# Kernel optimization log

Hardware: AMD Instinct MI355X
Metric: run time of the kernel (lower is better)

The kernel has to match this reference:

```python
import jax, jax.numpy as jnp
import numpy as np

N = 100000
E = 1600000
F_IN = 128
H = 128
C = 2


def setup_inputs() -> dict:
    key = jax.random.key(0)
    ks = jax.random.split(key, 12)
    s = lambda fan_in: 1.0 / np.sqrt(fan_in)
    inp = {
        "x": jax.random.normal(ks[0], (N, F_IN), dtype=jnp.float32),
        "edge_index": jax.random.randint(ks[1], (2, E), 0, N, dtype=jnp.int32),
        "edge_weight": jax.random.uniform(ks[2], (E,), dtype=jnp.float32),
        # first_lin: features_num -> hidden
        "W_first": jax.random.uniform(ks[3], (F_IN, H), minval=-s(F_IN), maxval=s(F_IN)),
        "b_first": jnp.zeros((H,), jnp.float32),
        # GRUCell (torch layout: [3*H, H] for ih and hh)
        "W_ih": jax.random.uniform(ks[4], (3 * H, H), minval=-s(H), maxval=s(H)),
        "b_ih": jax.random.uniform(ks[5], (3 * H,), minval=-s(H), maxval=s(H)),
        "W_hh": jax.random.uniform(ks[6], (3 * H, H), minval=-s(H), maxval=s(H)),
        "b_hh": jax.random.uniform(ks[7], (3 * H,), minval=-s(H), maxval=s(H)),
        # lin1: hidden -> hidden
        "W_lin1": jax.random.uniform(ks[8], (H, H), minval=-s(H), maxval=s(H)),
        "b_lin1": jnp.zeros((H,), jnp.float32),
        # out: hidden -> num_class
        "W_out": jax.random.uniform(ks[9], (H, C), minval=-s(H), maxval=s(H)),
        "b_out": jnp.zeros((C,), jnp.float32),
    }
    return inp


def _gated_conv(x, edge_index, edge_weight):
    # gather source node features, scale by edge weight, scatter-add to dst
    src, dst = edge_index[0], edge_index[1]
    msg = x[src] * edge_weight[:, None]           # [E, H]
    return jax.ops.segment_sum(msg, dst, num_segments=N)  # [N, H]


def _gru_cell(inp, hid, W_ih, b_ih, W_hh, b_hh):
    gi = inp @ W_ih.T + b_ih                      # [N, 3H]
    gh = hid @ W_hh.T + b_hh                      # [N, 3H]
    i_r, i_z, i_n = jnp.split(gi, 3, axis=-1)
    h_r, h_z, h_n = jnp.split(gh, 3, axis=-1)
    r = jax.nn.sigmoid(i_r + h_r)
    z = jax.nn.sigmoid(i_z + h_z)
    n = jnp.tanh(i_n + r * h_n)
    return (1.0 - z) * n + z * hid


def reference(x, edge_index, edge_weight, W_first, b_first, W_ih, b_ih,
              W_hh, b_hh, W_lin1, b_lin1, W_out, b_out):
    x = x @ W_first + b_first                     # [N, H] (dropout: eval mode no-op)
    h = x
    x = _gated_conv(x, edge_index, edge_weight)
    x = _gru_cell(x, h, W_ih, b_ih, W_hh, b_hh)
    x = x @ W_lin1 + b_lin1
    x = _gated_conv(x, edge_index, edge_weight)
    x = _gru_cell(x, h, W_ih, b_ih, W_hh, b_hh)
    logits = x @ W_out + b_out                    # [N, C]
    return jax.nn.log_softmax(logits, axis=-1)
```

## Files before the change

### kernel.cpp

```cpp
#include <hip/hip_runtime.h>
#include <hip/hip_bf16.h>

#define H 128
#define SCAN_T 256
#define SCAN_I 8
#define SCAN_CHUNK (SCAN_T * SCAN_I)

typedef __bf16 bf16_t;
typedef __attribute__((ext_vector_type(2))) __bf16 bf16x2;
typedef __attribute__((ext_vector_type(8))) __bf16 bf16x8;
typedef __attribute__((ext_vector_type(4))) float f32x4;

static_assert(sizeof(bf16x8) == 16, "bf16x8 must be 16 bytes");

__device__ inline bf16x8 load_a_frag_f32(const float* __restrict__ A, int row, int koff) {
    const float4* p = (const float4*)(A + (size_t)row * H + koff);
    float4 v0 = p[0], v1 = p[1];
    bf16x8 r;
    r[0] = (bf16_t)v0.x; r[1] = (bf16_t)v0.y; r[2] = (bf16_t)v0.z; r[3] = (bf16_t)v0.w;
    r[4] = (bf16_t)v1.x; r[5] = (bf16_t)v1.y; r[6] = (bf16_t)v1.z; r[7] = (bf16_t)v1.w;
    return r;
}

__global__ void prep_weights(const float* __restrict__ Wf,  const float* __restrict__ Wih,
                             const float* __restrict__ Whh, const float* __restrict__ Wl1,
                             bf16_t* __restrict__ wfT, bf16_t* __restrict__ wih,
                             bf16_t* __restrict__ whh, bf16_t* __restrict__ wl1T) {
    int i = blockIdx.x * blockDim.x + threadIdx.x;
    if (i < 128 * 128) {
        int c = i >> 7, k = i & 127;
        wfT[i]  = (bf16_t)Wf[k * 128 + c];
        wl1T[i] = (bf16_t)Wl1[k * 128 + c];
    }
    if (i < 384 * 128) {
        wih[i] = (bf16_t)Wih[i];
        whh[i] = (bf16_t)Whh[i];
    }
}

__global__ void hist_kernel(const int* __restrict__ ei, int* __restrict__ deg, int nE) {
    int e = blockIdx.x * blockDim.x + threadIdx.x;
    if (e < nE) atomicAdd(&deg[ei[nE + e]], 1);
}

__global__ __launch_bounds__(SCAN_T) void scan1_kernel(
    const int* __restrict__ deg, int* __restrict__ rowptr, int* __restrict__ bsum, int n) {
    __shared__ int s[SCAN_T];
    int base = blockIdx.x * SCAN_CHUNK + threadIdx.x * SCAN_I;
    int v[SCAN_I];
    int sum = 0;
    for (int j = 0; j < SCAN_I; ++j) {
        int idx = base + j;
        v[j] = (idx < n) ? deg[idx] : 0;
        sum += v[j];
    }
    s[threadIdx.x] = sum;
    __syncthreads();
    for (int off = 1; off < SCAN_T; off <<= 1) {
        int t = (threadIdx.x >= off) ? s[threadIdx.x - off] : 0;
        __syncthreads();
        s[threadIdx.x] += t;
        __syncthreads();
    }
    int run = s[threadIdx.x] - sum;
    for (int j = 0; j < SCAN_I; ++j) {
        int idx = base + j;
        if (idx < n) rowptr[idx] = run;
        run += v[j];
    }
    if (threadIdx.x == SCAN_T - 1) bsum[blockIdx.x] = s[SCAN_T - 1];
}

__global__ __launch_bounds__(SCAN_T) void scan2_kernel(int* __restrict__ bsum, int nb) {
    __shared__ int s[SCAN_T];
    int v = (threadIdx.x < nb) ? bsum[threadIdx.x] : 0;
    s[threadIdx.x] = v;
    __syncthreads();
    for (int off = 1; off < SCAN_T; off <<= 1) {
        int t = (threadIdx.x >= off) ? s[threadIdx.x - off] : 0;
        __syncthreads();
        s[threadIdx.x] += t;
        __syncthreads();
    }
    if (threadIdx.x < nb) bsum[threadIdx.x] = s[threadIdx.x] - v;
}

__global__ void scan3_kernel(int* __restrict__ rowptr, int* __restrict__ cursor,
                             const int* __restrict__ bsum, int n, int nE) {
    int idx = blockIdx.x * blockDim.x + threadIdx.x;
    if (idx < n) {
        int val = rowptr[idx] + bsum[idx / SCAN_CHUNK];
        rowptr[idx] = val;
        cursor[idx] = val;
    }
    if (idx == 0) rowptr[n] = nE;
}

__global__ void scatter_kernel(const int* __restrict__ ei, const float* __restrict__ ew,
                               int* __restrict__ cursor, int2* __restrict__ srcw, int nE) {
    int e = blockIdx.x * blockDim.x + threadIdx.x;
    if (e < nE) {
        int src = ei[e], dst = ei[nE + e];
        float w = ew[e];
        int pos = atomicAdd(&cursor[dst], 1);
        srcw[pos] = make_int2(src, __float_as_int(w));
    }
}

__device__ inline void conv_fma(float* acc, uint4 u, float w) {
    acc[0] += __uint_as_float(u.x << 16) * w;
    acc[1] += __uint_as_float(u.x & 0xffff0000u) * w;
    acc[2] += __uint_as_float(u.y << 16) * w;
    acc[3] += __uint_as_float(u.y & 0xffff0000u) * w;
    acc[4] += __uint_as_float(u.z << 16) * w;
    acc[5] += __uint_as_float(u.z & 0xffff0000u) * w;
    acc[6] += __uint_as_float(u.w << 16) * w;
    acc[7] += __uint_as_float(u.w & 0xffff0000u) * w;
}

__global__ __launch_bounds__(256) void conv_csr_kernel(
    const bf16_t* __restrict__ xb, const int* __restrict__ rowptr,
    const int2* __restrict__ srcw, bf16_t* __restrict__ agg, int n) {
    int lane = threadIdx.x & 63;
    int d = (blockIdx.x * blockDim.x + threadIdx.x) >> 6;
    if (d >= n) return;
    int q = lane >> 4;
    int l = lane & 15;
    int beg = rowptr[d], end = rowptr[d + 1];

    float acc[8];
    #pragma unroll
    for (int i = 0; i < 8; ++i) acc[i] = 0.f;

    int e = beg + q;
    for (; e + 4 < end; e += 8) {
        int2 sw0 = srcw[e];
        int2 sw1 = srcw[e + 4];
        uint4 u0 = *(const uint4*)(xb + (size_t)sw0.x * H + l * 8);
        uint4 u1 = *(const uint4*)(xb + (size_t)sw1.x * H + l * 8);
        conv_fma(acc, u0, __int_as_float(sw0.y));
        conv_fma(acc, u1, __int_as_float(sw1.y));
    }
    if (e < end) {
        int2 sw = srcw[e];
        uint4 u = *(const uint4*)(xb + (size_t)sw.x * H + l * 8);
        conv_fma(acc, u, __int_as_float(sw.y));
    }

    #pragma unroll
    for (int i = 0; i < 8; ++i) {
        acc[i] += __shfl_xor(acc[i], 16);
        acc[i] += __shfl_xor(acc[i], 32);
    }
    if (q == 0) {
        bf16x8 r;
        #pragma unroll
        for (int i = 0; i < 8; ++i) r[i] = (bf16_t)acc[i];
        *(bf16x8*)(agg + (size_t)d * H + l * 8) = r;
    }
}


__global__ __launch_bounds__(256) void lin_first_kernel(
    const float* __restrict__ A, const bf16_t* __restrict__ Bt,
    const float* __restrict__ bias, float* __restrict__ outf,
    bf16_t* __restrict__ outb, int n) {
    __shared__ __align__(16) unsigned char wlds[32768];
    int tid = threadIdx.x;
    int wid = tid >> 6, lane = tid & 63;
    int r0 = (blockIdx.x * 4 + wid) * 32;
    int lrow = lane & 15, lq = lane >> 4, lk8 = lq * 8;

    #pragma unroll
    for (int i = 0; i < 8; ++i) {
        int g = i * 256 + tid;
        int row = g >> 4, seg = g & 15;
        uint4 v = *(const uint4*)(Bt + row * 128 + seg * 8);
        *(uint4*)(&wlds[row * 256 + ((seg * 16) ^ ((row & 7) << 4))]) = v;
    }

    bf16x8 a[2][4];
    for (int rt = 0; rt < 2; ++rt) {
        int row = r0 + rt * 16 + lrow;
        if (row >= n) row = n - 1;
        for (int t = 0; t < 4; ++t) a[rt][t] = load_a_frag_f32(A, row, t * 32 + lk8);
    }
    __syncthreads();

    for (int ct = 0; ct < 8; ++ct) {
        int c0 = ct * 16;
        f32x4 acc0 = {0.f, 0.f, 0.f, 0.f}, acc1 = {0.f, 0.f, 0.f, 0.f};
        int rbase = (c0 + lrow) * 256;
        int sw = (lrow & 7) << 4;
        #pragma unroll
        for (int t = 0; t < 4; ++t) {
            bf16x8 b = *(const bf16x8*)(&wlds[rbase + ((t * 64 + lq * 16) ^ sw)]);
            acc0 = __builtin_amdgcn_mfma_f32_16x16x32_bf16(a[0][t], b, acc0, 0, 0, 0);
            acc1 = __builtin_amdgcn_mfma_f32_16x16x32_bf16(a[1][t], b, acc1, 0, 0, 0);
        }
        int col = c0 + lrow;
        float bv = bias[col];
        for (int r = 0; r < 4; ++r) {
            int row0 = r0 + lq * 4 + r;
            float v0 = acc0[r] + bv;
            if (row0 < n) { outf[(size_t)row0 * H + col] = v0; outb[(size_t)row0 * H + col] = (bf16_t)v0; }
            int row1 = row0 + 16;
            float v1 = acc1[r] + bv;
            if (row1 < n) { outf[(size_t)row1 * H + col] = v1; outb[(size_t)row1 * H + col] = (bf16_t)v1; }
        }
    }
}

__global__ __launch_bounds__(256) void lin_mid_kernel(
    const bf16_t* __restrict__ A, const bf16_t* __restrict__ Bt,
    const float* __restrict__ bias, bf16_t* __restrict__ out, int n) {
    __shared__ __align__(16) unsigned char wlds[32768];
    int tid = threadIdx.x;
    int wid = tid >> 6, lane = tid & 63;
    int r0 = (blockIdx.x * 4 + wid) * 32;
    int lrow = lane & 15, lq = lane >> 4, lk8 = lq * 8;

    #pragma unroll
    for (int i = 0; i < 8; ++i) {
        int g = i * 256 + tid;
        int row = g >> 4, seg = g & 15;
        uint4 v = *(const uint4*)(Bt + row * 128 + seg * 8);
        *(uint4*)(&wlds[row * 256 + ((seg * 16) ^ ((row & 7) << 4))]) = v;
    }

    bf16x8 a[2][4];
    for (int rt = 0; rt < 2; ++rt) {
        int row = r0 + rt * 16 + lrow;
        if (row >= n) row = n - 1;
        for (int t = 0; t < 4; ++t)
            a[rt][t] = *(const bf16x8*)(A + (size_t)row * H + t * 32 + lk8);
    }
    __syncthreads();

    for (int ct = 0; ct < 8; ++ct) {
        int c0 = ct * 16;
        f32x4 acc0 = {0.f, 0.f, 0.f, 0.f}, acc1 = {0.f, 0.f, 0.f, 0.f};
        int rbase = (c0 + lrow) * 256;
        int sw = (lrow & 7) << 4;
        #pragma unroll
        for (int t = 0; t < 4; ++t) {
            bf16x8 b = *(const bf16x8*)(&wlds[rbase + ((t * 64 + lq * 16) ^ sw)]);
            acc0 = __builtin_amdgcn_mfma_f32_16x16x32_bf16(a[0][t], b, acc0, 0, 0, 0);
            acc1 = __builtin_amdgcn_mfma_f32_16x16x32_bf16(a[1][t], b, acc1, 0, 0, 0);
        }
        int col = c0 + lrow;
        float bv = bias[col];
        for (int r = 0; r < 4; ++r) {
            int row0 = r0 + lq * 4 + r;
            if (row0 < n) out[(size_t)row0 * H + col] = (bf16_t)(acc0[r] + bv);
            int row1 = row0 + 16;
            if (row1 < n) out[(size_t)row1 * H + col] = (bf16_t)(acc1[r] + bv);
        }
    }
}

template<bool LOGITS>
__global__ __launch_bounds__(256) void gru_kernel(
    const bf16_t* __restrict__ inp, const bf16_t* __restrict__ hidb,
    const float* __restrict__ hidf,
    const bf16_t* __restrict__ Wih, const bf16_t* __restrict__ Whh,
    const float* __restrict__ bih, const float* __restrict__ bhh,
    bf16_t* __restrict__ out, const float* __restrict__ Wo,
    const float* __restrict__ bo, float* __restrict__ logits, int n) {
    __shared__ __align__(16) unsigned char wlds[2][6 * 4096];
    int tid = threadIdx.x;
    int wid = tid >> 6, lane = tid & 63;
    int r0 = (blockIdx.x * 4 + wid) * 32;
    int lrow = lane & 15, lq = lane >> 4, lk8 = lq * 8;

    int srow = tid >> 4;
    int sseg = tid & 15;
    int s_src_off = srow * 128 + sseg * 8;
    int s_lds_off = srow * 256 + ((sseg * 16) ^ ((srow & 7) << 4));

    uint4 streg[6];
    auto stage_load = [&](int ct) {
        const bf16_t* b0 = Wih + (size_t)(ct * 16) * 128;
        const bf16_t* b1 = Wih + (size_t)(128 + ct * 16) * 128;
        const bf16_t* b2 = Wih + (size_t)(256 + ct * 16) * 128;
        const bf16_t* b3 = Whh + (size_t)(ct * 16) * 128;
        const bf16_t* b4 = Whh + (size_t)(128 + ct * 16) * 128;
        const bf16_t* b5 = Whh + (size_t)(256 + ct * 16) * 128;
        streg[0] = *(const uint4*)(b0 + s_src_off);
        streg[1] = *(const uint4*)(b1 + s_src_off);
        streg[2] = *(const uint4*)(b2 + s_src_off);
        streg[3] = *(const uint4*)(b3 + s_src_off);
        streg[4] = *(const uint4*)(b4 + s_src_off);
        streg[5] = *(const uint4*)(b5 + s_src_off);
    };
    auto stage_write = [&](int buf) {
        #pragma unroll
        for (int s = 0; s < 6; ++s)
            *(uint4*)(&wlds[buf][s * 4096 + s_lds_off]) = streg[s];
    };

    bf16x8 ai[2][4], ah[2][4];
    for (int rt = 0; rt < 2; ++rt) {
        int row = r0 + rt * 16 + lrow;
        if (row >= n) row = n - 1;
        for (int t = 0; t < 4; ++t) {
            ai[rt][t] = *(const bf16x8*)(inp  + (size_t)row * H + t * 32 + lk8);
            ah[rt][t] = *(const bf16x8*)(hidb + (size_t)row * H + t * 32 + lk8);
        }
    }

    stage_load(0);
    stage_write(0);
    __syncthreads();

    float s0[2][4], s1[2][4];
    if (LOGITS) {
        for (int rt = 0; rt < 2; ++rt)
            for (int r = 0; r < 4; ++r) { s0[rt][r] = 0.f; s1[rt][r] = 0.f; }
    }

    for (int ct = 0; ct < 8; ++ct) {
        if (ct + 1 < 8) stage_load(ct + 1);
        const unsigned char* wb = wlds[ct & 1];
        int col = ct * 16 + lrow;

        f32x4 air[2], aiz[2], ain[2], ahr[2], ahz[2], ahn[2];
        for (int rt = 0; rt < 2; ++rt) {
            air[rt] = (f32x4){0.f,0.f,0.f,0.f}; aiz[rt] = (f32x4){0.f,0.f,0.f,0.f};
            ain[rt] = (f32x4){0.f,0.f,0.f,0.f}; ahr[rt] = (f32x4){0.f,0.f,0.f,0.f};
            ahz[rt] = (f32x4){0.f,0.f,0.f,0.f}; ahn[rt] = (f32x4){0.f,0.f,0.f,0.f};
        }
        int rbase = lrow * 256;
        int sw = (lrow & 7) << 4;
        #pragma unroll
        for (int t = 0; t < 4; ++t) {
            int roff = rbase + ((t * 64 + lq * 16) ^ sw);
            bf16x8 bir = *(const bf16x8*)(wb + 0 * 4096 + roff);
            bf16x8 biz = *(const bf16x8*)(wb + 1 * 4096 + roff);
            bf16x8 bin = *(const bf16x8*)(wb + 2 * 4096 + roff);
            bf16x8 bhr = *(const bf16x8*)(wb + 3 * 4096 + roff);
            bf16x8 bhz = *(const bf16x8*)(wb + 4 * 4096 + roff);
            bf16x8 bhn = *(const bf16x8*)(wb + 5 * 4096 + roff);
            for (int rt = 0; rt < 2; ++rt) {
                air[rt] = __builtin_amdgcn_mfma_f32_16x16x32_bf16(ai[rt][t], bir, air[rt], 0, 0, 0);
                aiz[rt] = __builtin_amdgcn_mfma_f32_16x16x32_bf16(ai[rt][t], biz, aiz[rt], 0, 0, 0);
                ain[rt] = __builtin_amdgcn_mfma_f32_16x16x32_bf16(ai[rt][t], bin, ain[rt], 0, 0, 0);
                ahr[rt] = __builtin_amdgcn_mfma_f32_16x16x32_bf16(ah[rt][t], bhr, ahr[rt], 0, 0, 0);
                ahz[rt] = __builtin_amdgcn_mfma_f32_16x16x32_bf16(ah[rt][t], bhz, ahz[rt], 0, 0, 0);
                ahn[rt] = __builtin_amdgcn_mfma_f32_16x16x32_bf16(ah[rt][t], bhn, ahn[rt], 0, 0, 0);
            }
        }

        float b_ir = bih[col], b_iz = bih[128 + col], b_in = bih[256 + col];
        float b_hr = bhh[col], b_hz = bhh[128 + col], b_hn = bhh[256 + col];
        float w0 = 0.f, w1 = 0.f;
        if (LOGITS) { float2 wv = *(const float2*)(Wo + col * 2); w0 = wv.x; w1 = wv.y; }
        for (int rt = 0; rt < 2; ++rt) {
            for (int r = 0; r < 4; ++r) {
                int row = r0 + rt * 16 + lq * 4 + r;
                float irv = air[rt][r] + b_ir, hrv = ahr[rt][r] + b_hr;
                float izv = aiz[rt][r] + b_iz, hzv = ahz[rt][r] + b_hz;
                float inv = ain[rt][r] + b_in, hnv = ahn[rt][r] + b_hn;
                float rg = 1.f / (1.f + __expf(-(irv + hrv)));
                float zg = 1.f / (1.f + __expf(-(izv + hzv)));
                float xx = inv + rg * hnv;
                float ng = 2.f / (1.f + __expf(-2.f * xx)) - 1.f;
                bool ok = (row < n);
                float hv = ok ? hidf[(size_t)row * H + col] : 0.f;
                float hout = (1.f - zg) * ng + zg * hv;
                if (LOGITS) {
                    s0[rt][r] += hout * w0;
                    s1[rt][r] += hout * w1;
                } else if (ok) {
                    out[(size_t)row * H + col] = (bf16_t)hout;
                }
            }
        }

        if (ct + 1 < 8) {
            stage_write((ct + 1) & 1);
            __syncthreads();
        }
    }

    if (LOGITS) {
        for (int m = 1; m < 16; m <<= 1) {
            for (int rt = 0; rt < 2; ++rt)
                for (int r = 0; r < 4; ++r) {
                    s0[rt][r] += __shfl_xor(s0[rt][r], m);
                    s1[rt][r] += __shfl_xor(s1[rt][r], m);
                }
        }
        if (lrow == 0) {
            float bo0 = bo[0], bo1 = bo[1];
            for (int rt = 0; rt < 2; ++rt)
                for (int r = 0; r < 4; ++r) {
                    int row = r0 + rt * 16 + lq * 4 + r;
                    if (row < n) {
                        float l0 = s0[rt][r] + bo0, l1 = s1[rt][r] + bo1;
                        float mx = fmaxf(l0, l1);
                        float lse = mx + __logf(__expf(l0 - mx) + __expf(l1 - mx));
                        logits[(size_t)row * 2]     = l0 - lse;
                        logits[(size_t)row * 2 + 1] = l1 - lse;
                    }
                }
        }
    }
}

extern "C" void kernel_launch(void* const* d_in, const int* in_sizes, int n_in,
                              void* d_out, int out_size, void* d_ws, size_t ws_size,
                              hipStream_t stream) {
    const float* x   = (const float*)d_in[0];
    const int*   ei  = (const int*)d_in[1];
    const float* ew  = (const float*)d_in[2];
    const float* Wf  = (const float*)d_in[3];
    const float* bf  = (const float*)d_in[4];
    const float* Wih = (const float*)d_in[5];
    const float* bih = (const float*)d_in[6];
    const float* Whh = (const float*)d_in[7];
    const float* bhh = (const float*)d_in[8];
    const float* Wl1 = (const float*)d_in[9];
    const float* bl1 = (const float*)d_in[10];
    const float* Wo  = (const float*)d_in[11];
    const float* bo  = (const float*)d_in[12];

    int n  = in_sizes[0] / H;
    int nE = in_sizes[2];

    float* hbuf   = (float*)d_ws;
    bf16_t* hbufb = (bf16_t*)(hbuf + (size_t)n * H);
    bf16_t* b1b   = hbufb + (size_t)n * H;
    bf16_t* b2b   = b1b + (size_t)n * H;
    bf16_t* wfT   = b2b + (size_t)n * H;
    bf16_t* wih   = wfT + 128 * 128;
    bf16_t* whh   = wih + 384 * 128;
    bf16_t* wl1T  = whh + 384 * 128;
    int* deg    = (int*)(wl1T + 128 * 128);
    int* rowptr = deg + n;
    int* cursor = rowptr + (n + 1);
    int2* srcw  = (int2*)((char*)(cursor + n) + ((size_t)(-(intptr_t)(cursor + n)) & 7));

    int gemmGrid = (n + 127) / 128;
    int nScanBlocks = (n + SCAN_CHUNK - 1) / SCAN_CHUNK;

    prep_weights<<<192, 256, 0, stream>>>(Wf, Wih, Whh, Wl1, wfT, wih, whh, wl1T);
    hipMemsetAsync(deg, 0, (size_t)n * sizeof(int), stream);
    hist_kernel<<<(nE + 255) / 256, 256, 0, stream>>>(ei, deg, nE);
    scan1_kernel<<<nScanBlocks, SCAN_T, 0, stream>>>(deg, rowptr, cursor, n);
    scan2_kernel<<<1, SCAN_T, 0, stream>>>(cursor, nScanBlocks);
    scan3_kernel<<<(n + 255) / 256, 256, 0, stream>>>(rowptr, deg, cursor, n, nE);
    scatter_kernel<<<(nE + 255) / 256, 256, 0, stream>>>(ei, ew, deg, srcw, nE);

    lin_first_kernel<<<gemmGrid, 256, 0, stream>>>(x, wfT, bf, hbuf, hbufb, n);
    conv_csr_kernel<<<(n + 3) / 4, 256, 0, stream>>>(hbufb, rowptr, srcw, b1b, n);
    gru_kernel<false><<<gemmGrid, 256, 0, stream>>>(b1b, hbufb, hbuf, wih, whh, bih, bhh,
                                                    b1b, nullptr, nullptr, nullptr, n);
    lin_mid_kernel<<<gemmGrid, 256, 0, stream>>>(b1b, wl1T, bl1, b2b, n);
    conv_csr_kernel<<<(n + 3) / 4, 256, 0, stream>>>(b2b, rowptr, srcw, b1b, n);
    gru_kernel<true><<<gemmGrid, 256, 0, stream>>>(b1b, hbufb, hbuf, wih, whh, bih, bhh,
                                                   nullptr, Wo, bo, (float*)d_out, n);
}
```

Baseline: 539.1 us.

## Drop fp32 hidden buffer, pull hidden via identity MFMA, partition scatter by dst

The first linear layer now writes only a bf16 copy of the hidden state. The GRU kernels recover the hidden value in accumulator layout with an identity-matrix MFMA on the already-loaded bf16 fragments, so the fp32 hidden store and reload are gone, at the cost of bf16 precision for the z*h term. The GRU weight staging drops the double-buffered register prefetch in favour of a single LDS buffer with two barriers per column tile. The CSR scatter is split across 8 destination slices, each grid-striding over all edges, so atomics to a slice stay localized, but the destination array is read 8 times.

```diff
diff --git a/kernel.cpp b/kernel.cpp
--- a/kernel.cpp
+++ b/kernel.cpp
@@ -96,14 +96,21 @@
     if (idx == 0) rowptr[n] = nE;
 }
 
-__global__ void scatter_kernel(const int* __restrict__ ei, const float* __restrict__ ew,
-                               int* __restrict__ cursor, int2* __restrict__ srcw, int nE) {
-    int e = blockIdx.x * blockDim.x + threadIdx.x;
-    if (e < nE) {
-        int src = ei[e], dst = ei[nE + e];
-        float w = ew[e];
-        int pos = atomicAdd(&cursor[dst], 1);
-        srcw[pos] = make_int2(src, __float_as_int(w));
+__global__ __launch_bounds__(256) void scatter_kernel(
+    const int* __restrict__ ei, const float* __restrict__ ew,
+    int* __restrict__ cursor, int2* __restrict__ srcw, int nE, int n) {
+    int r = blockIdx.x & 7;
+    int nslice = n >> 3;
+    int lo = r * nslice;
+    int hi = (r == 7) ? n : lo + nslice;
+    int chunk = blockIdx.x >> 3;
+    int nchunk = gridDim.x >> 3;
+    for (int e = chunk * 256 + threadIdx.x; e < nE; e += nchunk * 256) {
+        int dst = ei[nE + e];
+        if (dst >= lo && dst < hi) {
+            int pos = atomicAdd(&cursor[dst], 1);
+            srcw[pos] = make_int2(ei[e], __float_as_int(ew[e]));
+        }
     }
 }
 
@@ -163,8 +170,7 @@
 
 __global__ __launch_bounds__(256) void lin_first_kernel(
     const float* __restrict__ A, const bf16_t* __restrict__ Bt,
-    const float* __restrict__ bias, float* __restrict__ outf,
-    bf16_t* __restrict__ outb, int n) {
+    const float* __restrict__ bias, bf16_t* __restrict__ outb, int n) {
     __shared__ __align__(16) unsigned char wlds[32768];
     int tid = threadIdx.x;
     int wid = tid >> 6, lane = tid & 63;
@@ -202,11 +208,9 @@
         float bv = bias[col];
         for (int r = 0; r < 4; ++r) {
             int row0 = r0 + lq * 4 + r;
-            float v0 = acc0[r] + bv;
-            if (row0 < n) { outf[(size_t)row0 * H + col] = v0; outb[(size_t)row0 * H + col] = (bf16_t)v0; }
+            if (row0 < n) outb[(size_t)row0 * H + col] = (bf16_t)(acc0[r] + bv);
             int row1 = row0 + 16;
-            float v1 = acc1[r] + bv;
-            if (row1 < n) { outf[(size_t)row1 * H + col] = v1; outb[(size_t)row1 * H + col] = (bf16_t)v1; }
+            if (row1 < n) outb[(size_t)row1 * H + col] = (bf16_t)(acc1[r] + bv);
         }
     }
 }
@@ -262,42 +266,19 @@
 template<bool LOGITS>
 __global__ __launch_bounds__(256) void gru_kernel(
     const bf16_t* __restrict__ inp, const bf16_t* __restrict__ hidb,
-    const float* __restrict__ hidf,
     const bf16_t* __restrict__ Wih, const bf16_t* __restrict__ Whh,
     const float* __restrict__ bih, const float* __restrict__ bhh,
     bf16_t* __restrict__ out, const float* __restrict__ Wo,
     const float* __restrict__ bo, float* __restrict__ logits, int n) {
-    __shared__ __align__(16) unsigned char wlds[2][6 * 4096];
+    __shared__ __align__(16) unsigned char wlds[6 * 4096];
     int tid = threadIdx.x;
     int wid = tid >> 6, lane = tid & 63;
     int r0 = (blockIdx.x * 4 + wid) * 32;
     int lrow = lane & 15, lq = lane >> 4, lk8 = lq * 8;
 
-    int srow = tid >> 4;
-    int sseg = tid & 15;
-    int s_src_off = srow * 128 + sseg * 8;
-    int s_lds_off = srow * 256 + ((sseg * 16) ^ ((srow & 7) << 4));
-
-    uint4 streg[6];
-    auto stage_load = [&](int ct) {
-        const bf16_t* b0 = Wih + (size_t)(ct * 16) * 128;
-        const bf16_t* b1 = Wih + (size_t)(128 + ct * 16) * 128;
-        const bf16_t* b2 = Wih + (size_t)(256 + ct * 16) * 128;
-        const bf16_t* b3 = Whh + (size_t)(ct * 16) * 128;
-        const bf16_t* b4 = Whh + (size_t)(128 + ct * 16) * 128;
-        const bf16_t* b5 = Whh + (size_t)(256 + ct * 16) * 128;
-        streg[0] = *(const uint4*)(b0 + s_src_off);
-        streg[1] = *(const uint4*)(b1 + s_src_off);
-        streg[2] = *(const uint4*)(b2 + s_src_off);
-        streg[3] = *(const uint4*)(b3 + s_src_off);
-        streg[4] = *(const uint4*)(b4 + s_src_off);
-        streg[5] = *(const uint4*)(b5 + s_src_off);
-    };
-    auto stage_write = [&](int buf) {
-        #pragma unroll
-        for (int s = 0; s < 6; ++s)
-            *(uint4*)(&wlds[buf][s * 4096 + s_lds_off]) = streg[s];
-    };
+    int srow = tid >> 4, sseg = tid & 15;
+    int s_src = srow * 128 + sseg * 8;
+    int s_lds = srow * 256 + ((sseg * 16) ^ ((srow & 7) << 4));
 
     bf16x8 ai[2][4], ah[2][4];
     for (int rt = 0; rt < 2; ++rt) {
@@ -309,10 +290,6 @@
         }
     }
 
-    stage_load(0);
-    stage_write(0);
-    __syncthreads();
-
     float s0[2][4], s1[2][4];
     if (LOGITS) {
         for (int rt = 0; rt < 2; ++rt)
@@ -320,10 +297,22 @@
     }
 
     for (int ct = 0; ct < 8; ++ct) {
-        if (ct + 1 < 8) stage_load(ct + 1);
-        const unsigned char* wb = wlds[ct & 1];
+        uint4 u0 = *(const uint4*)(Wih + (size_t)(0 * 128 + ct * 16) * 128 + s_src);
+        uint4 u1 = *(const uint4*)(Wih + (size_t)(1 * 128 + ct * 16) * 128 + s_src);
+        uint4 u2 = *(const uint4*)(Wih + (size_t)(2 * 128 + ct * 16) * 128 + s_src);
+        uint4 u3 = *(const uint4*)(Whh + (size_t)(0 * 128 + ct * 16) * 128 + s_src);
+        uint4 u4 = *(const uint4*)(Whh + (size_t)(1 * 128 + ct * 16) * 128 + s_src);
+        uint4 u5 = *(const uint4*)(Whh + (size_t)(2 * 128 + ct * 16) * 128 + s_src);
+        __syncthreads();
+        *(uint4*)(&wlds[0 * 4096 + s_lds]) = u0;
+        *(uint4*)(&wlds[1 * 4096 + s_lds]) = u1;
+        *(uint4*)(&wlds[2 * 4096 + s_lds]) = u2;
+        *(uint4*)(&wlds[3 * 4096 + s_lds]) = u3;
+        *(uint4*)(&wlds[4 * 4096 + s_lds]) = u4;
+        *(uint4*)(&wlds[5 * 4096 + s_lds]) = u5;
+        __syncthreads();
+
         int col = ct * 16 + lrow;
-
         f32x4 air[2], aiz[2], ain[2], ahr[2], ahz[2], ahn[2];
         for (int rt = 0; rt < 2; ++rt) {
             air[rt] = (f32x4){0.f,0.f,0.f,0.f}; aiz[rt] = (f32x4){0.f,0.f,0.f,0.f};
@@ -335,12 +324,12 @@
         #pragma unroll
         for (int t = 0; t < 4; ++t) {
             int roff = rbase + ((t * 64 + lq * 16) ^ sw);
-            bf16x8 bir = *(const bf16x8*)(wb + 0 * 4096 + roff);
-            bf16x8 biz = *(const bf16x8*)(wb + 1 * 4096 + roff);
-            bf16x8 bin = *(const bf16x8*)(wb + 2 * 4096 + roff);
-            bf16x8 bhr = *(const bf16x8*)(wb + 3 * 4096 + roff);
-            bf16x8 bhz = *(const bf16x8*)(wb + 4 * 4096 + roff);
-            bf16x8 bhn = *(const bf16x8*)(wb + 5 * 4096 + roff);
+            bf16x8 bir = *(const bf16x8*)(&wlds[0 * 4096 + roff]);
+            bf16x8 biz = *(const bf16x8*)(&wlds[1 * 4096 + roff]);
+            bf16x8 bin = *(const bf16x8*)(&wlds[2 * 4096 + roff]);
+            bf16x8 bhr = *(const bf16x8*)(&wlds[3 * 4096 + roff]);
+            bf16x8 bhz = *(const bf16x8*)(&wlds[4 * 4096 + roff]);
+            bf16x8 bhn = *(const bf16x8*)(&wlds[5 * 4096 + roff]);
             for (int rt = 0; rt < 2; ++rt) {
                 air[rt] = __builtin_amdgcn_mfma_f32_16x16x32_bf16(ai[rt][t], bir, air[rt], 0, 0, 0);
                 aiz[rt] = __builtin_amdgcn_mfma_f32_16x16x32_bf16(ai[rt][t], biz, aiz[rt], 0, 0, 0);
@@ -349,6 +338,18 @@
                 ahz[rt] = __builtin_amdgcn_mfma_f32_16x16x32_bf16(ah[rt][t], bhz, ahz[rt], 0, 0, 0);
                 ahn[rt] = __builtin_amdgcn_mfma_f32_16x16x32_bf16(ah[rt][t], bhn, ahn[rt], 0, 0, 0);
             }
+        }
+
+        int idx = ((ct & 1) << 4) | lrow;
+        bf16x8 bid;
+        #pragma unroll
+        for (int j = 0; j < 8; ++j)
+            bid[j] = (bf16_t)((lq == (idx >> 3) && j == (idx & 7)) ? 1.f : 0.f);
+        int tct = ct >> 1;
+        f32x4 hc[2];
+        for (int rt = 0; rt < 2; ++rt) {
+            f32x4 z = {0.f, 0.f, 0.f, 0.f};
+            hc[rt] = __builtin_amdgcn_mfma_f32_16x16x32_bf16(ah[rt][tct], bid, z, 0, 0, 0);
         }
 
         float b_ir = bih[col], b_iz = bih[128 + col], b_in = bih[256 + col];
@@ -365,21 +366,15 @@
                 float zg = 1.f / (1.f + __expf(-(izv + hzv)));
                 float xx = inv + rg * hnv;
                 float ng = 2.f / (1.f + __expf(-2.f * xx)) - 1.f;
-                bool ok = (row < n);
-                float hv = ok ? hidf[(size_t)row * H + col] : 0.f;
+                float hv = hc[rt][r];
                 float hout = (1.f - zg) * ng + zg * hv;
                 if (LOGITS) {
                     s0[rt][r] += hout * w0;
                     s1[rt][r] += hout * w1;
-                } else if (ok) {
+                } else if (row < n) {
                     out[(size_t)row * H + col] = (bf16_t)hout;
                 }
             }
-        }
-
-        if (ct + 1 < 8) {
-            stage_write((ct + 1) & 1);
-            __syncthreads();
         }
     }
 
@@ -428,8 +423,7 @@
     int n  = in_sizes[0] / H;
     int nE = in_sizes[2];
 
-    float* hbuf   = (float*)d_ws;
-    bf16_t* hbufb = (bf16_t*)(hbuf + (size_t)n * H);
+    bf16_t* hbufb = (bf16_t*)d_ws;
     bf16_t* b1b   = hbufb + (size_t)n * H;
     bf16_t* b2b   = b1b + (size_t)n * H;
     bf16_t* wfT   = b2b + (size_t)n * H;
@@ -450,14 +444,14 @@
     scan1_kernel<<<nScanBlocks, SCAN_T, 0, stream>>>(deg, rowptr, cursor, n);
     scan2_kernel<<<1, SCAN_T, 0, stream>>>(cursor, nScanBlocks);
     scan3_kernel<<<(n + 255) / 256, 256, 0, stream>>>(rowptr, deg, cursor, n, nE);
-    scatter_kernel<<<(nE + 255) / 256, 256, 0, stream>>>(ei, ew, deg, srcw, nE);
-
-    lin_first_kernel<<<gemmGrid, 256, 0, stream>>>(x, wfT, bf, hbuf, hbufb, n);
+    scatter_kernel<<<2048, 256, 0, stream>>>(ei, ew, deg, srcw, nE, n);
+
+    lin_first_kernel<<<gemmGrid, 256, 0, stream>>>(x, wfT, bf, hbufb, n);
     conv_csr_kernel<<<(n + 3) / 4, 256, 0, stream>>>(hbufb, rowptr, srcw, b1b, n);
-    gru_kernel<false><<<gemmGrid, 256, 0, stream>>>(b1b, hbufb, hbuf, wih, whh, bih, bhh,
+    gru_kernel<false><<<gemmGrid, 256, 0, stream>>>(b1b, hbufb, wih, whh, bih, bhh,
                                                     b1b, nullptr, nullptr, nullptr, n);
     lin_mid_kernel<<<gemmGrid, 256, 0, stream>>>(b1b, wl1T, bl1, b2b, n);
     conv_csr_kernel<<<(n + 3) / 4, 256, 0, stream>>>(b2b, rowptr, srcw, b1b, n);
-    gru_kernel<true><<<gemmGrid, 256, 0, stream>>>(b1b, hbufb, hbuf, wih, whh, bih, bhh,
+    gru_kernel<true><<<gemmGrid, 256, 0, stream>>>(b1b, hbufb, wih, whh, bih, bhh,
                                                    nullptr, Wo, bo, (float*)d_out, n);
 }
```

Result: slower. 735.6 us (+36.4%).
